# Optimization experiments

Measured on AMD Instinct MI355X. Metric: run time of the kernel, lower is better.

Reference implementation:

```python
import jax, jax.numpy as jnp
import numpy as np

B, N, K, H = 4, 1024, 48, 128
E = 128          # edge feature dim; num_in = E + H = 256
FF = 4 * H       # dense feedforward width
EPS = 1e-5
SCALE = 30.0


def gelu(x):
    return jax.nn.gelu(x, approximate=False)


def linear(x, w, b):
    # torch Linear: w is [out, in]
    return x @ w.T + b


def layer_norm(x, g, b):
    mu = jnp.mean(x, axis=-1, keepdims=True)
    var = jnp.var(x, axis=-1, keepdims=True)
    return (x - mu) * jax.lax.rsqrt(var + EPS) * g + b


def gather_nodes(nodes, idx):
    # nodes [B,N,H], idx [B,N,K] -> [B,N,K,H]
    b, n, k = idx.shape
    flat = idx.reshape(b, n * k, 1)
    return jnp.take_along_axis(nodes, flat, axis=1).reshape(b, n, k, -1)


def setup_inputs():
    key = jax.random.key(0)
    ks = jax.random.split(key, 24)
    s = 0.05
    inp = {
        "h_V": jax.random.normal(ks[0], (B, N, H), jnp.float32),
        "h_E": jax.random.normal(ks[1], (B, N, K, E), jnp.float32),
        "E_idx": jax.random.randint(ks[2], (B, N, K), 0, N, jnp.int64),
        "mask_V": jnp.ones((B, N), jnp.float32),
        "mask_attend": jnp.ones((B, N, K), jnp.float32),
        # node-update message MLP (input dim H + E + H = 3H here)
        "W1_w": jax.random.normal(ks[3], (H, H + E + H), jnp.float32) * s,
        "W1_b": jnp.zeros((H,), jnp.float32),
        "W2_w": jax.random.normal(ks[4], (H, H), jnp.float32) * s,
        "W2_b": jnp.zeros((H,), jnp.float32),
        "W3_w": jax.random.normal(ks[5], (H, H), jnp.float32) * s,
        "W3_b": jnp.zeros((H,), jnp.float32),
        # edge-update message MLP
        "W11_w": jax.random.normal(ks[6], (H, H + E + H), jnp.float32) * s,
        "W11_b": jnp.zeros((H,), jnp.float32),
        "W12_w": jax.random.normal(ks[7], (H, H), jnp.float32) * s,
        "W12_b": jnp.zeros((H,), jnp.float32),
        "W13_w": jax.random.normal(ks[8], (H, H), jnp.float32) * s,
        "W13_b": jnp.zeros((H,), jnp.float32),
        # layer norms
        "ln0_g": jnp.ones((H,), jnp.float32), "ln0_b": jnp.zeros((H,), jnp.float32),
        "ln1_g": jnp.ones((H,), jnp.float32), "ln1_b": jnp.zeros((H,), jnp.float32),
        "ln2_g": jnp.ones((H,), jnp.float32), "ln2_b": jnp.zeros((H,), jnp.float32),
        # position-wise feedforward
        "Win_w": jax.random.normal(ks[9], (FF, H), jnp.float32) * s,
        "Win_b": jnp.zeros((FF,), jnp.float32),
        "Wout_w": jax.random.normal(ks[10], (H, FF), jnp.float32) * s,
        "Wout_b": jnp.zeros((H,), jnp.float32),
        # ReZero residual weight (init 0 in the module; nonzero for testing)
        "resweight": jax.random.normal(ks[11], (1,), jnp.float32) * 0.1,
    }
    return inp


def reference(h_V, h_E, E_idx, mask_V, mask_attend,
              W1_w, W1_b, W2_w, W2_b, W3_w, W3_b,
              W11_w, W11_b, W12_w, W12_b, W13_w, W13_b,
              ln0_g, ln0_b, ln1_g, ln1_b, ln2_g, ln2_b,
              Win_w, Win_b, Wout_w, Wout_b, resweight):
    # ---- node update (pre-norm, ReZero-scaled residual), dropout=eval ----
    residual = h_V
    hVn = layer_norm(h_V, ln0_g, ln0_b)
    h_nbr = gather_nodes(hVn, E_idx)                              # [B,N,K,H]
    h_EV = jnp.concatenate(
        [jnp.broadcast_to(hVn[:, :, None, :], (B, N, K, H)), h_E, h_nbr], axis=-1)
    h_message = linear(gelu(linear(gelu(linear(h_EV, W1_w, W1_b)), W2_w, W2_b)), W3_w, W3_b)
    h_message = mask_attend[..., None] * h_message
    dh = jnp.sum(h_message, axis=-2) / SCALE
    h_V = residual + dh * resweight

    # ---- position-wise feedforward ----
    residual = h_V
    hVn = layer_norm(h_V, ln1_g, ln1_b)
    dh = linear(gelu(linear(hVn, Win_w, Win_b)), Wout_w, Wout_b)
    h_V = residual + dh * resweight
    h_V = mask_V[..., None] * h_V

    # ---- edge update (no ReZero scaling on this branch) ----
    residual = h_E
    hEn = layer_norm(h_E, ln2_g, ln2_b)
    h_nbr = gather_nodes(h_V, E_idx)
    h_EV = jnp.concatenate(
        [jnp.broadcast_to(h_V[:, :, None, :], (B, N, K, H)), hEn, h_nbr], axis=-1)
    h_message = linear(gelu(linear(gelu(linear(h_EV, W11_w, W11_b)), W12_w, W12_b)), W13_w, W13_b)
    h_E = residual + h_message

    return h_V, h_E
```

## Files before the change

kernel.cpp:

```cpp
#include <hip/hip_runtime.h>
#include <hip/hip_bf16.h>

#define BB 4
#define NN 1024
#define KK 48
#define HH 128
#define EE 128
#define IN3 384
#define FF 512
#define ST 132

typedef __attribute__((ext_vector_type(8))) short bf16x8;
typedef __attribute__((ext_vector_type(4))) float f32x4;

#define MFMA(a, b, c) __builtin_amdgcn_mfma_f32_16x16x32_bf16((a), (b), (c), 0, 0, 0)

__device__ __forceinline__ float bf2f(ushort u) {
    union { uint i; float f; } v; v.i = ((uint)u) << 16; return v.f;
}
__device__ __forceinline__ uint cvtpk(float a, float b) {
    uint r;
    asm("v_cvt_pk_bf16_f32 %0, %1, %2" : "=v"(r) : "v"(a), "v"(b));
    return r;
}
__device__ __forceinline__ ushort f2bf1(float v) {
    return (ushort)cvtpk(v, v);
}
__device__ __forceinline__ float wsum(float x) {
    #pragma unroll
    for (int o = 32; o; o >>= 1) x += __shfl_xor(x, o, 64);
    return x;
}
__device__ __forceinline__ float gelu_f(float x) {
    float t = x * fmaf(x * x, 0.044715f, 1.0f);
    float a = fminf(t * 2.3022061f, 50.0f);
    float z;
    asm("v_exp_f32 %0, %1" : "=v"(z) : "v"(a));
    float r;
    asm("v_rcp_f32 %0, %1" : "=v"(r) : "v"(z + 1.0f));
    return x * z * r;
}

__global__ __launch_bounds__(256) void k_cvt8(
    const float* __restrict__ s0, const float* __restrict__ s1,
    const float* __restrict__ s2, const float* __restrict__ s3,
    const float* __restrict__ s4, const float* __restrict__ s5,
    const float* __restrict__ s6, const float* __restrict__ s7,
    ushort* __restrict__ d0, ushort* __restrict__ d1,
    ushort* __restrict__ d2, ushort* __restrict__ d3,
    ushort* __restrict__ d4, ushort* __restrict__ d5,
    ushort* __restrict__ d6, ushort* __restrict__ d7) {
    int i = blockIdx.x * 256 + threadIdx.x;
    const float* s; ushort* d; int base;
    if      (i < 12288) { s = s0; d = d0; base = 0; }
    else if (i < 16384) { s = s1; d = d1; base = 12288; }
    else if (i < 20480) { s = s2; d = d2; base = 16384; }
    else if (i < 32768) { s = s3; d = d3; base = 20480; }
    else if (i < 36864) { s = s4; d = d4; base = 32768; }
    else if (i < 40960) { s = s5; d = d5; base = 36864; }
    else if (i < 57344) { s = s6; d = d6; base = 40960; }
    else                { s = s7; d = d7; base = 57344; }
    int j = i - base;
    float4 v = ((const float4*)s)[j];
    uint2 o;
    o.x = cvtpk(v.x, v.y);
    o.y = cvtpk(v.z, v.w);
    ((uint2*)d)[j] = o;
}

__global__ __launch_bounds__(256) void k_ln0(const float* __restrict__ hV,
                                             const float* __restrict__ g,
                                             const float* __restrict__ bta,
                                             ushort* __restrict__ out) {
    int row = blockIdx.x * 4 + (threadIdx.x >> 6);
    int l = threadIdx.x & 63;
    const float* src = hV + (size_t)row * HH;
    float x0 = src[l], x1 = src[l + 64];
    float s = wsum(x0 + x1);
    float q = wsum(x0 * x0 + x1 * x1);
    float mu = s * (1.0f / 128.0f);
    float rstd = rsqrtf(q * (1.0f / 128.0f) - mu * mu + 1e-5f);
    ushort* dst = out + (size_t)row * HH;
    dst[l]      = f2bf1((x0 - mu) * rstd * g[l]      + bta[l]);
    dst[l + 64] = f2bf1((x1 - mu) * rstd * g[l + 64] + bta[l + 64]);
}

__global__ __launch_bounds__(256, 6) void k_node(
    const float* __restrict__ hV, const float* __restrict__ hE,
    const int* __restrict__ Eidx, const float* __restrict__ maskAtt,
    const ushort* __restrict__ W1w, const float* __restrict__ W1b,
    const ushort* __restrict__ W2w, const float* __restrict__ W2b,
    const ushort* __restrict__ W3w, const float* __restrict__ W3b,
    const float* __restrict__ resw,
    const ushort* __restrict__ hVn,
    float* __restrict__ outHVp) {

    __shared__ ushort sB[KK * ST];
    __shared__ ushort sC[KK * ST];
    __shared__ float  sMask[KK];
    __shared__ float  sCol[128];

    const int t = threadIdx.x;
    const int w = t >> 6;
    const int lane = t & 63;
    const int bn = blockIdx.x;
    const int b  = bn >> 10;
    const size_t nbase = (size_t)bn * HH;
    const int r16 = lane & 15, g4 = lane >> 4;

    int myidx[3];
    #pragma unroll
    for (int mm = 0; mm < 3; mm++) myidx[mm] = Eidx[bn * KK + mm * 16 + r16];
    if (t < KK) sMask[t] = maskAtt[bn * KK + t];

    f32x4 acc[3][2];
    #pragma unroll
    for (int mm = 0; mm < 3; mm++)
        #pragma unroll
        for (int nn = 0; nn < 2; nn++) acc[mm][nn] = (f32x4){0.f, 0.f, 0.f, 0.f};

    const ushort* Wp = W1w + (w * 32 + r16) * IN3 + g4 * 8;

    {
        const ushort* nb = hVn + (size_t)b * NN * HH + g4 * 8;
        #pragma unroll
        for (int kt = 0; kt < 4; kt++) {
            bf16x8 b0 = *(const bf16x8*)(Wp + 256 + kt * 32);
            bf16x8 b1 = *(const bf16x8*)(Wp + 16 * IN3 + 256 + kt * 32);
            #pragma unroll
            for (int mm = 0; mm < 3; mm++) {
                bf16x8 a = *(const bf16x8*)(nb + (size_t)myidx[mm] * HH + kt * 32);
                acc[mm][0] = MFMA(a, b0, acc[mm][0]);
                acc[mm][1] = MFMA(a, b1, acc[mm][1]);
            }
        }
    }
    {
        const float* hEp = hE + (size_t)bn * KK * EE;
        #pragma unroll
        for (int kt = 0; kt < 4; kt++) {
            bf16x8 b0 = *(const bf16x8*)(Wp + 128 + kt * 32);
            bf16x8 b1 = *(const bf16x8*)(Wp + 16 * IN3 + 128 + kt * 32);
            #pragma unroll
            for (int mm = 0; mm < 3; mm++) {
                const float* p = hEp + (mm * 16 + r16) * EE + kt * 32 + g4 * 8;
                float4 f0 = *(const float4*)(p);
                float4 f1 = *(const float4*)(p + 4);
                union { uint u[4]; bf16x8 v; } a;
                a.u[0] = cvtpk(f0.x, f0.y); a.u[1] = cvtpk(f0.z, f0.w);
                a.u[2] = cvtpk(f1.x, f1.y); a.u[3] = cvtpk(f1.z, f1.w);
                acc[mm][0] = MFMA(a.v, b0, acc[mm][0]);
                acc[mm][1] = MFMA(a.v, b1, acc[mm][1]);
            }
        }
    }
    {
        const ushort* sp = hVn + nbase + g4 * 8;
        #pragma unroll
        for (int kt = 0; kt < 4; kt++) {
            bf16x8 aself = *(const bf16x8*)(sp + kt * 32);
            bf16x8 b0 = *(const bf16x8*)(Wp + kt * 32);
            bf16x8 b1 = *(const bf16x8*)(Wp + 16 * IN3 + kt * 32);
            #pragma unroll
            for (int mm = 0; mm < 3; mm++) {
                acc[mm][0] = MFMA(aself, b0, acc[mm][0]);
                acc[mm][1] = MFMA(aself, b1, acc[mm][1]);
            }
        }
    }
    #pragma unroll
    for (int nn = 0; nn < 2; nn++) {
        int col = w * 32 + nn * 16 + r16;
        float bb = W1b[col];
        #pragma unroll
        for (int mm = 0; mm < 3; mm++)
            #pragma unroll
            for (int r = 0; r < 4; r++)
                sB[(mm * 16 + g4 * 4 + r) * ST + col] = f2bf1(gelu_f(acc[mm][nn][r] + bb));
    }
    __syncthreads();

    f32x4 acc2[3][2];
    #pragma unroll
    for (int mm = 0; mm < 3; mm++)
        #pragma unroll
        for (int nn = 0; nn < 2; nn++) acc2[mm][nn] = (f32x4){0.f, 0.f, 0.f, 0.f};
    {
        const ushort* Wp2 = W2w + (w * 32 + r16) * HH + g4 * 8;
        #pragma unroll
        for (int kt = 0; kt < 4; kt++) {
            bf16x8 b0 = *(const bf16x8*)(Wp2 + kt * 32);
            bf16x8 b1 = *(const bf16x8*)(Wp2 + 16 * HH + kt * 32);
            #pragma unroll
            for (int mm = 0; mm < 3; mm++) {
                bf16x8 a = *(const bf16x8*)&sB[(mm * 16 + r16) * ST + kt * 32 + g4 * 8];
                acc2[mm][0] = MFMA(a, b0, acc2[mm][0]);
                acc2[mm][1] = MFMA(a, b1, acc2[mm][1]);
            }
        }
    }
    #pragma unroll
    for (int nn = 0; nn < 2; nn++) {
        int col = w * 32 + nn * 16 + r16;
        float bb = W2b[col];
        #pragma unroll
        for (int mm = 0; mm < 3; mm++)
            #pragma unroll
            for (int r = 0; r < 4; r++)
                sC[(mm * 16 + g4 * 4 + r) * ST + col] = f2bf1(gelu_f(acc2[mm][nn][r] + bb));
    }
    __syncthreads();

    f32x4 acc3[3][2];
    #pragma unroll
    for (int mm = 0; mm < 3; mm++)
        #pragma unroll
        for (int nn = 0; nn < 2; nn++) acc3[mm][nn] = (f32x4){0.f, 0.f, 0.f, 0.f};
    {
        const ushort* Wp3 = W3w + (w * 32 + r16) * HH + g4 * 8;
        #pragma unroll
        for (int kt = 0; kt < 4; kt++) {
            bf16x8 b0 = *(const bf16x8*)(Wp3 + kt * 32);
            bf16x8 b1 = *(const bf16x8*)(Wp3 + 16 * HH + kt * 32);
            #pragma unroll
            for (int mm = 0; mm < 3; mm++) {
                bf16x8 a = *(const bf16x8*)&sC[(mm * 16 + r16) * ST + kt * 32 + g4 * 8];
                acc3[mm][0] = MFMA(a, b0, acc3[mm][0]);
                acc3[mm][1] = MFMA(a, b1, acc3[mm][1]);
            }
        }
    }
    {
        float b3a = W3b[w * 32 + r16];
        float b3b = W3b[w * 32 + 16 + r16];
        float s0 = 0.f, s1 = 0.f;
        #pragma unroll
        for (int mm = 0; mm < 3; mm++)
            #pragma unroll
            for (int r = 0; r < 4; r++) {
                float mk = sMask[mm * 16 + g4 * 4 + r];
                s0 += (acc3[mm][0][r] + b3a) * mk;
                s1 += (acc3[mm][1][r] + b3b) * mk;
            }
        s0 += __shfl_xor(s0, 16, 64); s0 += __shfl_xor(s0, 32, 64);
        s1 += __shfl_xor(s1, 16, 64); s1 += __shfl_xor(s1, 32, 64);
        if (g4 == 0) {
            sCol[w * 32 + r16]      = s0;
            sCol[w * 32 + 16 + r16] = s1;
        }
    }
    __syncthreads();

    if (t < 128) {
        float rw = resw[0];
        outHVp[nbase + t] = hV[nbase + t] + sCol[t] * (1.0f / 30.0f) * rw;
    }
}

__global__ __launch_bounds__(256, 4) void k_ffn(
    const float* __restrict__ maskV,
    const float* __restrict__ ln1g, const float* __restrict__ ln1b,
    const ushort* __restrict__ Winw, const float* __restrict__ Winb,
    const ushort* __restrict__ Woutw, const float* __restrict__ Woutb,
    const float* __restrict__ resw,
    const float* __restrict__ hVp,
    float* __restrict__ outV,
    ushort* __restrict__ hV2b) {

    __shared__ float  sHVp[16 * 132];
    __shared__ ushort sX[16 * 136];
    __shared__ ushort sY[16 * 520];
    __shared__ float  sMk[16];

    const int t = threadIdx.x;
    const int w = t >> 6;
    const int lane = t & 63;
    const int nb = blockIdx.x * 16;
    const int r16 = lane & 15, g4 = lane >> 4;

    #pragma unroll
    for (int i = 0; i < 8; i++) {
        int e = t + i * 256;
        sHVp[(e >> 7) * 132 + (e & 127)] = hVp[(size_t)nb * HH + e];
    }
    if (t < 16) sMk[t] = maskV[nb + t];
    __syncthreads();

    #pragma unroll
    for (int i = 0; i < 4; i++) {
        int row = w * 4 + i;
        float x0 = sHVp[row * 132 + lane], x1 = sHVp[row * 132 + 64 + lane];
        float s = wsum(x0 + x1);
        float q = wsum(x0 * x0 + x1 * x1);
        float mu = s * (1.0f / 128.0f);
        float rstd = rsqrtf(q * (1.0f / 128.0f) - mu * mu + 1e-5f);
        sX[row * 136 + lane]      = f2bf1((x0 - mu) * rstd * ln1g[lane]      + ln1b[lane]);
        sX[row * 136 + 64 + lane] = f2bf1((x1 - mu) * rstd * ln1g[64 + lane] + ln1b[64 + lane]);
    }
    __syncthreads();

    f32x4 acc1[8];
    #pragma unroll
    for (int nn = 0; nn < 8; nn++) acc1[nn] = (f32x4){0.f, 0.f, 0.f, 0.f};
    bf16x8 a1[4];
    #pragma unroll
    for (int kt = 0; kt < 4; kt++)
        a1[kt] = *(const bf16x8*)&sX[r16 * 136 + kt * 32 + g4 * 8];
    #pragma unroll
    for (int nn = 0; nn < 8; nn++) {
        const ushort* Wq = Winw + (w * 128 + nn * 16 + r16) * HH + g4 * 8;
        #pragma unroll
        for (int kt = 0; kt < 4; kt++)
            acc1[nn] = MFMA(a1[kt], *(const bf16x8*)(Wq + kt * 32), acc1[nn]);
    }
    #pragma unroll
    for (int nn = 0; nn < 8; nn++) {
        int col = w * 128 + nn * 16 + r16;
        float bb = Winb[col];
        #pragma unroll
        for (int r = 0; r < 4; r++)
            sY[(g4 * 4 + r) * 520 + col] = f2bf1(gelu_f(acc1[nn][r] + bb));
    }
    __syncthreads();

    f32x4 acc2[2];
    acc2[0] = (f32x4){0.f, 0.f, 0.f, 0.f};
    acc2[1] = (f32x4){0.f, 0.f, 0.f, 0.f};
    {
        const ushort* Wq = Woutw + (w * 32 + r16) * FF + g4 * 8;
        #pragma unroll 4
        for (int kt = 0; kt < 16; kt++) {
            bf16x8 a = *(const bf16x8*)&sY[r16 * 520 + kt * 32 + g4 * 8];
            acc2[0] = MFMA(a, *(const bf16x8*)(Wq + kt * 32), acc2[0]);
            acc2[1] = MFMA(a, *(const bf16x8*)(Wq + 16 * FF + kt * 32), acc2[1]);
        }
    }
    float rw = resw[0];
    #pragma unroll
    for (int nn = 0; nn < 2; nn++) {
        int col = w * 32 + nn * 16 + r16;
        float bb = Woutb[col];
        #pragma unroll
        for (int r = 0; r < 4; r++) {
            int row = g4 * 4 + r;
            float out = sHVp[row * 132 + col] + (acc2[nn][r] + bb) * rw;
            out *= sMk[row];
            outV[(size_t)(nb + row) * HH + col] = out;
            hV2b[(size_t)(nb + row) * HH + col] = f2bf1(out);
        }
    }
}

__global__ __launch_bounds__(256, 6) void k_edge(
    const float* __restrict__ hE, const int* __restrict__ Eidx,
    const ushort* __restrict__ W11w, const float* __restrict__ W11b,
    const ushort* __restrict__ W12w, const float* __restrict__ W12b,
    const ushort* __restrict__ W13w, const float* __restrict__ W13b,
    const float* __restrict__ ln2g, const float* __restrict__ ln2b,
    const ushort* __restrict__ hV2b,
    float* __restrict__ outE) {

    __shared__ ushort sM[KK * ST];
    __shared__ ushort sB[KK * ST];

    const int t = threadIdx.x;
    const int w = t >> 6;
    const int lane = t & 63;
    const int bn = blockIdx.x;
    const int b  = bn >> 10;
    const size_t nbase = (size_t)bn * HH;
    const size_t ebase = (size_t)bn * KK * EE;
    const int r16 = lane & 15, g4 = lane >> 4;

    int myidx[3];
    #pragma unroll
    for (int mm = 0; mm < 3; mm++) myidx[mm] = Eidx[bn * KK + mm * 16 + r16];

    {
        float g0 = ln2g[2 * lane], g1 = ln2g[2 * lane + 1];
        float c0 = ln2b[2 * lane], c1 = ln2b[2 * lane + 1];
        #pragma unroll 3
        for (int i = 0; i < 12; i++) {
            int k = w + i * 4;
            float2 pr = ((const float2*)(hE + ebase + (size_t)k * EE))[lane];
            float x0 = pr.x, x1 = pr.y;
            float s = wsum(x0 + x1);
            float q = wsum(x0 * x0 + x1 * x1);
            float mu = s * (1.0f / 128.0f);
            float rstd = rsqrtf(q * (1.0f / 128.0f) - mu * mu + 1e-5f);
            uint packed = cvtpk((x0 - mu) * rstd * g0 + c0, (x1 - mu) * rstd * g1 + c1);
            *(uint*)&sM[k * ST + 2 * lane] = packed;
        }
    }
    __syncthreads();

    f32x4 acc[3][2];
    #pragma unroll
    for (int mm = 0; mm < 3; mm++)
        #pragma unroll
        for (int nn = 0; nn < 2; nn++) acc[mm][nn] = (f32x4){0.f, 0.f, 0.f, 0.f};

    const ushort* Wp = W11w + (w * 32 + r16) * IN3 + g4 * 8;
    {
        const ushort* nb = hV2b + (size_t)b * NN * HH + g4 * 8;
        #pragma unroll
        for (int kt = 0; kt < 4; kt++) {
            bf16x8 b0 = *(const bf16x8*)(Wp + 256 + kt * 32);
            bf16x8 b1 = *(const bf16x8*)(Wp + 16 * IN3 + 256 + kt * 32);
            #pragma unroll
            for (int mm = 0; mm < 3; mm++) {
                bf16x8 a = *(const bf16x8*)(nb + (size_t)myidx[mm] * HH + kt * 32);
                acc[mm][0] = MFMA(a, b0, acc[mm][0]);
                acc[mm][1] = MFMA(a, b1, acc[mm][1]);
            }
        }
    }
    {
        const ushort* sp = hV2b + nbase + g4 * 8;
        #pragma unroll
        for (int kt = 0; kt < 4; kt++) {
            bf16x8 aself = *(const bf16x8*)(sp + kt * 32);
            bf16x8 b0 = *(const bf16x8*)(Wp + kt * 32);
            bf16x8 b1 = *(const bf16x8*)(Wp + 16 * IN3 + kt * 32);
            #pragma unroll
            for (int mm = 0; mm < 3; mm++) {
                acc[mm][0] = MFMA(aself, b0, acc[mm][0]);
                acc[mm][1] = MFMA(aself, b1, acc[mm][1]);
            }
        }
    }
    #pragma unroll
    for (int kt = 0; kt < 4; kt++) {
        bf16x8 b0 = *(const bf16x8*)(Wp + 128 + kt * 32);
        bf16x8 b1 = *(const bf16x8*)(Wp + 16 * IN3 + 128 + kt * 32);
        #pragma unroll
        for (int mm = 0; mm < 3; mm++) {
            bf16x8 a = *(const bf16x8*)&sM[(mm * 16 + r16) * ST + kt * 32 + g4 * 8];
            acc[mm][0] = MFMA(a, b0, acc[mm][0]);
            acc[mm][1] = MFMA(a, b1, acc[mm][1]);
        }
    }
    #pragma unroll
    for (int nn = 0; nn < 2; nn++) {
        int col = w * 32 + nn * 16 + r16;
        float bb = W11b[col];
        #pragma unroll
        for (int mm = 0; mm < 3; mm++)
            #pragma unroll
            for (int r = 0; r < 4; r++)
                sB[(mm * 16 + g4 * 4 + r) * ST + col] = f2bf1(gelu_f(acc[mm][nn][r] + bb));
    }
    __syncthreads();

    f32x4 acc2[3][2];
    #pragma unroll
    for (int mm = 0; mm < 3; mm++)
        #pragma unroll
        for (int nn = 0; nn < 2; nn++) acc2[mm][nn] = (f32x4){0.f, 0.f, 0.f, 0.f};
    {
        const ushort* Wp2 = W12w + (w * 32 + r16) * HH + g4 * 8;
        #pragma unroll
        for (int kt = 0; kt < 4; kt++) {
            bf16x8 b0 = *(const bf16x8*)(Wp2 + kt * 32);
            bf16x8 b1 = *(const bf16x8*)(Wp2 + 16 * HH + kt * 32);
            #pragma unroll
            for (int mm = 0; mm < 3; mm++) {
                bf16x8 a = *(const bf16x8*)&sB[(mm * 16 + r16) * ST + kt * 32 + g4 * 8];
                acc2[mm][0] = MFMA(a, b0, acc2[mm][0]);
                acc2[mm][1] = MFMA(a, b1, acc2[mm][1]);
            }
        }
    }
    #pragma unroll
    for (int nn = 0; nn < 2; nn++) {
        int col = w * 32 + nn * 16 + r16;
        float bb = W12b[col];
        #pragma unroll
        for (int mm = 0; mm < 3; mm++)
            #pragma unroll
            for (int r = 0; r < 4; r++)
                sM[(mm * 16 + g4 * 4 + r) * ST + col] = f2bf1(gelu_f(acc2[mm][nn][r] + bb));
    }
    __syncthreads();

    f32x4 acc3[3][2];
    #pragma unroll
    for (int mm = 0; mm < 3; mm++)
        #pragma unroll
        for (int nn = 0; nn < 2; nn++) acc3[mm][nn] = (f32x4){0.f, 0.f, 0.f, 0.f};
    {
        const ushort* Wp3 = W13w + (w * 32 + r16) * HH + g4 * 8;
        #pragma unroll
        for (int kt = 0; kt < 4; kt++) {
            bf16x8 b0 = *(const bf16x8*)(Wp3 + kt * 32);
            bf16x8 b1 = *(const bf16x8*)(Wp3 + 16 * HH + kt * 32);
            #pragma unroll
            for (int mm = 0; mm < 3; mm++) {
                bf16x8 a = *(const bf16x8*)&sM[(mm * 16 + r16) * ST + kt * 32 + g4 * 8];
                acc3[mm][0] = MFMA(a, b0, acc3[mm][0]);
                acc3[mm][1] = MFMA(a, b1, acc3[mm][1]);
            }
        }
    }
    #pragma unroll
    for (int nn = 0; nn < 2; nn++) {
        int col = w * 32 + nn * 16 + r16;
        float bb = W13b[col];
        #pragma unroll
        for (int mm = 0; mm < 3; mm++)
            #pragma unroll
            for (int r = 0; r < 4; r++)
                sB[(mm * 16 + g4 * 4 + r) * ST + col] = f2bf1(acc3[mm][nn][r] + bb);
    }
    __syncthreads();

    {
        const float4* esrc = (const float4*)(hE + ebase);
        float4* edst = (float4*)(outE + ebase);
        #pragma unroll
        for (int i = 0; i < 6; i++) {
            int c = t + i * 256;
            int k = c >> 5, cp = (c & 31) * 4;
            float4 ev = esrc[c];
            const ushort* mrow = &sB[k * ST + cp];
            float4 ov;
            ov.x = ev.x + bf2f(mrow[0]);
            ov.y = ev.y + bf2f(mrow[1]);
            ov.z = ev.z + bf2f(mrow[2]);
            ov.w = ev.w + bf2f(mrow[3]);
            edst[c] = ov;
        }
    }
}

extern "C" void kernel_launch(void* const* d_in, const int* in_sizes, int n_in,
                              void* d_out, int out_size, void* d_ws, size_t ws_size,
                              hipStream_t stream) {
    const float* hV      = (const float*)d_in[0];
    const float* hE      = (const float*)d_in[1];
    const int*   Eidx    = (const int*)d_in[2];
    const float* maskV   = (const float*)d_in[3];
    const float* maskAtt = (const float*)d_in[4];
    const float* W1w  = (const float*)d_in[5];
    const float* W1b  = (const float*)d_in[6];
    const float* W2w  = (const float*)d_in[7];
    const float* W2b  = (const float*)d_in[8];
    const float* W3w  = (const float*)d_in[9];
    const float* W3b  = (const float*)d_in[10];
    const float* W11w = (const float*)d_in[11];
    const float* W11b = (const float*)d_in[12];
    const float* W12w = (const float*)d_in[13];
    const float* W12b = (const float*)d_in[14];
    const float* W13w = (const float*)d_in[15];
    const float* W13b = (const float*)d_in[16];
    const float* ln0g = (const float*)d_in[17];
    const float* ln0b = (const float*)d_in[18];
    const float* ln1g = (const float*)d_in[19];
    const float* ln1b = (const float*)d_in[20];
    const float* ln2g = (const float*)d_in[21];
    const float* ln2b = (const float*)d_in[22];
    const float* Winw  = (const float*)d_in[23];
    const float* Winb  = (const float*)d_in[24];
    const float* Woutw = (const float*)d_in[25];
    const float* Woutb = (const float*)d_in[26];
    const float* resw  = (const float*)d_in[27];

    float* outV = (float*)d_out;
    float* outE = outV + (size_t)BB * NN * HH;

    char* wsb = (char*)d_ws;
    ushort* wsHVn = (ushort*)wsb;
    float*  wHVp  = (float*)(wsb + (1 << 20));
    ushort* wHV2b = (ushort*)(wsb + 3 * (1 << 20));
    ushort* wW1   = (ushort*)(wsb + 4 * (1 << 20));
    ushort* wW2   = wW1  + HH * IN3;
    ushort* wW3   = wW2  + HH * HH;
    ushort* wW11  = wW3  + HH * HH;
    ushort* wW12  = wW11 + HH * IN3;
    ushort* wW13  = wW12 + HH * HH;
    ushort* wWin  = wW13 + HH * HH;
    ushort* wWout = wWin + FF * HH;

    k_cvt8<<<dim3(288), dim3(256), 0, stream>>>(
        W1w, W2w, W3w, W11w, W12w, W13w, Winw, Woutw,
        wW1, wW2, wW3, wW11, wW12, wW13, wWin, wWout);

    k_ln0<<<dim3(BB * NN / 4), dim3(256), 0, stream>>>(hV, ln0g, ln0b, wsHVn);
    k_node<<<dim3(BB * NN), dim3(256), 0, stream>>>(
        hV, hE, Eidx, maskAtt,
        wW1, W1b, wW2, W2b, wW3, W3b, resw, wsHVn, wHVp);
    k_ffn<<<dim3(BB * NN / 16), dim3(256), 0, stream>>>(
        maskV, ln1g, ln1b, wWin, Winb, wWout, Woutb, resw, wHVp, outV, wHV2b);
    k_edge<<<dim3(BB * NN), dim3(256), 0, stream>>>(
        hE, Eidx, wW11, W11b, wW12, W12b, wW13, W13b,
        ln2g, ln2b, wHV2b, outE);
}
```

Before: 281.9 us.

## Process two nodes per block in node and edge kernels with shared LDS buffer

Each block of k_node and k_edge now handles two nodes (96 edge rows) instead of one, so every weight fragment loaded from global memory feeds twice as many MFMAs. The two LDS staging buffers are merged into one buffer that is reused in place, with extra barriers added. The edge kernel's final residual add now writes directly from registers to global memory instead of staging through LDS. Costs include doubled accumulator register pressure, lower launch-bounds occupancy (4 blocks instead of 6), half as many blocks, and strided scalar global stores in the edge epilogue.

```diff
diff --git a/kernel.cpp b/kernel.cpp
--- a/kernel.cpp
+++ b/kernel.cpp
@@ -85,7 +85,7 @@
     dst[l + 64] = f2bf1((x1 - mu) * rstd * g[l + 64] + bta[l + 64]);
 }
 
-__global__ __launch_bounds__(256, 6) void k_node(
+__global__ __launch_bounds__(256, 4) void k_node(
     const float* __restrict__ hV, const float* __restrict__ hE,
     const int* __restrict__ Eidx, const float* __restrict__ maskAtt,
     const ushort* __restrict__ W1w, const float* __restrict__ W1b,
@@ -95,32 +95,49 @@
     const ushort* __restrict__ hVn,
     float* __restrict__ outHVp) {
 
-    __shared__ ushort sB[KK * ST];
-    __shared__ ushort sC[KK * ST];
-    __shared__ float  sMask[KK];
-    __shared__ float  sCol[128];
+    __shared__ ushort buf[96 * ST];
+    __shared__ float  sMask[96];
+    __shared__ float  sCol[256];
 
     const int t = threadIdx.x;
     const int w = t >> 6;
     const int lane = t & 63;
-    const int bn = blockIdx.x;
-    const int b  = bn >> 10;
-    const size_t nbase = (size_t)bn * HH;
+    const int np = blockIdx.x * 2;
+    const int b  = np >> 10;
     const int r16 = lane & 15, g4 = lane >> 4;
 
-    int myidx[3];
-    #pragma unroll
-    for (int mm = 0; mm < 3; mm++) myidx[mm] = Eidx[bn * KK + mm * 16 + r16];
-    if (t < KK) sMask[t] = maskAtt[bn * KK + t];
-
-    f32x4 acc[3][2];
-    #pragma unroll
-    for (int mm = 0; mm < 3; mm++)
-        #pragma unroll
-        for (int nn = 0; nn < 2; nn++) acc[mm][nn] = (f32x4){0.f, 0.f, 0.f, 0.f};
-
-    const ushort* Wp = W1w + (w * 32 + r16) * IN3 + g4 * 8;
-
+    int myidx[6];
+    #pragma unroll
+    for (int mt = 0; mt < 6; mt++)
+        myidx[mt] = Eidx[np * KK + mt * 16 + r16];
+    if (t < 96) sMask[t] = maskAtt[np * KK + t];
+
+    f32x4 acc[6][2];
+    #pragma unroll
+    for (int mt = 0; mt < 6; mt++) {
+        acc[mt][0] = (f32x4){0.f, 0.f, 0.f, 0.f};
+        acc[mt][1] = (f32x4){0.f, 0.f, 0.f, 0.f};
+    }
+
+    const ushort* Wp  = W1w + (w * 32 + r16) * IN3 + g4 * 8;
+    const float*  hE0 = hE + (size_t)np * KK * EE;
+
+    #pragma unroll
+    for (int kt = 0; kt < 4; kt++) {
+        bf16x8 b0 = *(const bf16x8*)(Wp + 128 + kt * 32);
+        bf16x8 b1 = *(const bf16x8*)(Wp + 16 * IN3 + 128 + kt * 32);
+        #pragma unroll
+        for (int mt = 0; mt < 6; mt++) {
+            const float* p = hE0 + (size_t)(mt * 16 + r16) * EE + kt * 32 + g4 * 8;
+            float4 f0 = *(const float4*)(p);
+            float4 f1 = *(const float4*)(p + 4);
+            union { uint u[4]; bf16x8 v; } a;
+            a.u[0] = cvtpk(f0.x, f0.y); a.u[1] = cvtpk(f0.z, f0.w);
+            a.u[2] = cvtpk(f1.x, f1.y); a.u[3] = cvtpk(f1.z, f1.w);
+            acc[mt][0] = MFMA(a.v, b0, acc[mt][0]);
+            acc[mt][1] = MFMA(a.v, b1, acc[mt][1]);
+        }
+    }
     {
         const ushort* nb = hVn + (size_t)b * NN * HH + g4 * 8;
         #pragma unroll
@@ -128,43 +145,27 @@
             bf16x8 b0 = *(const bf16x8*)(Wp + 256 + kt * 32);
             bf16x8 b1 = *(const bf16x8*)(Wp + 16 * IN3 + 256 + kt * 32);
             #pragma unroll
-            for (int mm = 0; mm < 3; mm++) {
-                bf16x8 a = *(const bf16x8*)(nb + (size_t)myidx[mm] * HH + kt * 32);
-                acc[mm][0] = MFMA(a, b0, acc[mm][0]);
-                acc[mm][1] = MFMA(a, b1, acc[mm][1]);
-            }
-        }
-    }
-    {
-        const float* hEp = hE + (size_t)bn * KK * EE;
-        #pragma unroll
-        for (int kt = 0; kt < 4; kt++) {
-            bf16x8 b0 = *(const bf16x8*)(Wp + 128 + kt * 32);
-            bf16x8 b1 = *(const bf16x8*)(Wp + 16 * IN3 + 128 + kt * 32);
-            #pragma unroll
-            for (int mm = 0; mm < 3; mm++) {
-                const float* p = hEp + (mm * 16 + r16) * EE + kt * 32 + g4 * 8;
-                float4 f0 = *(const float4*)(p);
-                float4 f1 = *(const float4*)(p + 4);
-                union { uint u[4]; bf16x8 v; } a;
-                a.u[0] = cvtpk(f0.x, f0.y); a.u[1] = cvtpk(f0.z, f0.w);
-                a.u[2] = cvtpk(f1.x, f1.y); a.u[3] = cvtpk(f1.z, f1.w);
-                acc[mm][0] = MFMA(a.v, b0, acc[mm][0]);
-                acc[mm][1] = MFMA(a.v, b1, acc[mm][1]);
-            }
-        }
-    }
-    {
-        const ushort* sp = hVn + nbase + g4 * 8;
-        #pragma unroll
-        for (int kt = 0; kt < 4; kt++) {
-            bf16x8 aself = *(const bf16x8*)(sp + kt * 32);
+            for (int mt = 0; mt < 6; mt++) {
+                bf16x8 a = *(const bf16x8*)(nb + (size_t)myidx[mt] * HH + kt * 32);
+                acc[mt][0] = MFMA(a, b0, acc[mt][0]);
+                acc[mt][1] = MFMA(a, b1, acc[mt][1]);
+            }
+        }
+    }
+    {
+        const ushort* sp0 = hVn + (size_t)np * HH + g4 * 8;
+        const ushort* sp1 = sp0 + HH;
+        #pragma unroll
+        for (int kt = 0; kt < 4; kt++) {
+            bf16x8 a0 = *(const bf16x8*)(sp0 + kt * 32);
+            bf16x8 a1 = *(const bf16x8*)(sp1 + kt * 32);
             bf16x8 b0 = *(const bf16x8*)(Wp + kt * 32);
             bf16x8 b1 = *(const bf16x8*)(Wp + 16 * IN3 + kt * 32);
             #pragma unroll
-            for (int mm = 0; mm < 3; mm++) {
-                acc[mm][0] = MFMA(aself, b0, acc[mm][0]);
-                acc[mm][1] = MFMA(aself, b1, acc[mm][1]);
+            for (int mt = 0; mt < 6; mt++) {
+                bf16x8 a = (mt < 3) ? a0 : a1;
+                acc[mt][0] = MFMA(a, b0, acc[mt][0]);
+                acc[mt][1] = MFMA(a, b1, acc[mt][1]);
             }
         }
     }
@@ -173,18 +174,19 @@
         int col = w * 32 + nn * 16 + r16;
         float bb = W1b[col];
         #pragma unroll
-        for (int mm = 0; mm < 3; mm++)
+        for (int mt = 0; mt < 6; mt++)
             #pragma unroll
             for (int r = 0; r < 4; r++)
-                sB[(mm * 16 + g4 * 4 + r) * ST + col] = f2bf1(gelu_f(acc[mm][nn][r] + bb));
-    }
-    __syncthreads();
-
-    f32x4 acc2[3][2];
-    #pragma unroll
-    for (int mm = 0; mm < 3; mm++)
-        #pragma unroll
-        for (int nn = 0; nn < 2; nn++) acc2[mm][nn] = (f32x4){0.f, 0.f, 0.f, 0.f};
+                buf[(mt * 16 + g4 * 4 + r) * ST + col] = f2bf1(gelu_f(acc[mt][nn][r] + bb));
+    }
+    __syncthreads();
+
+    f32x4 acc2[6][2];
+    #pragma unroll
+    for (int mt = 0; mt < 6; mt++) {
+        acc2[mt][0] = (f32x4){0.f, 0.f, 0.f, 0.f};
+        acc2[mt][1] = (f32x4){0.f, 0.f, 0.f, 0.f};
+    }
     {
         const ushort* Wp2 = W2w + (w * 32 + r16) * HH + g4 * 8;
         #pragma unroll
@@ -192,30 +194,32 @@
             bf16x8 b0 = *(const bf16x8*)(Wp2 + kt * 32);
             bf16x8 b1 = *(const bf16x8*)(Wp2 + 16 * HH + kt * 32);
             #pragma unroll
-            for (int mm = 0; mm < 3; mm++) {
-                bf16x8 a = *(const bf16x8*)&sB[(mm * 16 + r16) * ST + kt * 32 + g4 * 8];
-                acc2[mm][0] = MFMA(a, b0, acc2[mm][0]);
-                acc2[mm][1] = MFMA(a, b1, acc2[mm][1]);
-            }
-        }
-    }
+            for (int mt = 0; mt < 6; mt++) {
+                bf16x8 a = *(const bf16x8*)&buf[(mt * 16 + r16) * ST + kt * 32 + g4 * 8];
+                acc2[mt][0] = MFMA(a, b0, acc2[mt][0]);
+                acc2[mt][1] = MFMA(a, b1, acc2[mt][1]);
+            }
+        }
+    }
+    __syncthreads();
     #pragma unroll
     for (int nn = 0; nn < 2; nn++) {
         int col = w * 32 + nn * 16 + r16;
         float bb = W2b[col];
         #pragma unroll
-        for (int mm = 0; mm < 3; mm++)
+        for (int mt = 0; mt < 6; mt++)
             #pragma unroll
             for (int r = 0; r < 4; r++)
-                sC[(mm * 16 + g4 * 4 + r) * ST + col] = f2bf1(gelu_f(acc2[mm][nn][r] + bb));
-    }
-    __syncthreads();
-
-    f32x4 acc3[3][2];
-    #pragma unroll
-    for (int mm = 0; mm < 3; mm++)
-        #pragma unroll
-        for (int nn = 0; nn < 2; nn++) acc3[mm][nn] = (f32x4){0.f, 0.f, 0.f, 0.f};
+                buf[(mt * 16 + g4 * 4 + r) * ST + col] = f2bf1(gelu_f(acc2[mt][nn][r] + bb));
+    }
+    __syncthreads();
+
+    f32x4 acc3[6][2];
+    #pragma unroll
+    for (int mt = 0; mt < 6; mt++) {
+        acc3[mt][0] = (f32x4){0.f, 0.f, 0.f, 0.f};
+        acc3[mt][1] = (f32x4){0.f, 0.f, 0.f, 0.f};
+    }
     {
         const ushort* Wp3 = W3w + (w * 32 + r16) * HH + g4 * 8;
         #pragma unroll
@@ -223,37 +227,45 @@
             bf16x8 b0 = *(const bf16x8*)(Wp3 + kt * 32);
             bf16x8 b1 = *(const bf16x8*)(Wp3 + 16 * HH + kt * 32);
             #pragma unroll
-            for (int mm = 0; mm < 3; mm++) {
-                bf16x8 a = *(const bf16x8*)&sC[(mm * 16 + r16) * ST + kt * 32 + g4 * 8];
-                acc3[mm][0] = MFMA(a, b0, acc3[mm][0]);
-                acc3[mm][1] = MFMA(a, b1, acc3[mm][1]);
+            for (int mt = 0; mt < 6; mt++) {
+                bf16x8 a = *(const bf16x8*)&buf[(mt * 16 + r16) * ST + kt * 32 + g4 * 8];
+                acc3[mt][0] = MFMA(a, b0, acc3[mt][0]);
+                acc3[mt][1] = MFMA(a, b1, acc3[mt][1]);
             }
         }
     }
     {
         float b3a = W3b[w * 32 + r16];
         float b3b = W3b[w * 32 + 16 + r16];
-        float s0 = 0.f, s1 = 0.f;
-        #pragma unroll
-        for (int mm = 0; mm < 3; mm++)
+        float s0a = 0.f, s0b = 0.f, s1a = 0.f, s1b = 0.f;
+        #pragma unroll
+        for (int mt = 0; mt < 6; mt++)
             #pragma unroll
             for (int r = 0; r < 4; r++) {
-                float mk = sMask[mm * 16 + g4 * 4 + r];
-                s0 += (acc3[mm][0][r] + b3a) * mk;
-                s1 += (acc3[mm][1][r] + b3b) * mk;
-            }
-        s0 += __shfl_xor(s0, 16, 64); s0 += __shfl_xor(s0, 32, 64);
-        s1 += __shfl_xor(s1, 16, 64); s1 += __shfl_xor(s1, 32, 64);
+                int row = mt * 16 + g4 * 4 + r;
+                float mk = sMask[row];
+                float v0 = (acc3[mt][0][r] + b3a) * mk;
+                float v1 = (acc3[mt][1][r] + b3b) * mk;
+                if (mt < 3) { s0a += v0; s0b += v1; }
+                else        { s1a += v0; s1b += v1; }
+            }
+        s0a += __shfl_xor(s0a, 16, 64); s0a += __shfl_xor(s0a, 32, 64);
+        s0b += __shfl_xor(s0b, 16, 64); s0b += __shfl_xor(s0b, 32, 64);
+        s1a += __shfl_xor(s1a, 16, 64); s1a += __shfl_xor(s1a, 32, 64);
+        s1b += __shfl_xor(s1b, 16, 64); s1b += __shfl_xor(s1b, 32, 64);
         if (g4 == 0) {
-            sCol[w * 32 + r16]      = s0;
-            sCol[w * 32 + 16 + r16] = s1;
-        }
-    }
-    __syncthreads();
-
-    if (t < 128) {
+            sCol[w * 32 + r16]            = s0a;
+            sCol[w * 32 + 16 + r16]       = s0b;
+            sCol[128 + w * 32 + r16]      = s1a;
+            sCol[128 + w * 32 + 16 + r16] = s1b;
+        }
+    }
+    __syncthreads();
+
+    {
         float rw = resw[0];
-        outHVp[nbase + t] = hV[nbase + t] + sCol[t] * (1.0f / 30.0f) * rw;
+        size_t o = (size_t)np * HH + t;
+        outHVp[o] = hV[o] + sCol[t] * (1.0f / 30.0f) * rw;
     }
 }
 
@@ -351,7 +363,7 @@
     }
 }
 
-__global__ __launch_bounds__(256, 6) void k_edge(
+__global__ __launch_bounds__(256, 4) void k_edge(
     const float* __restrict__ hE, const int* __restrict__ Eidx,
     const ushort* __restrict__ W11w, const float* __restrict__ W11b,
     const ushort* __restrict__ W12w, const float* __restrict__ W12b,
@@ -360,46 +372,45 @@
     const ushort* __restrict__ hV2b,
     float* __restrict__ outE) {
 
-    __shared__ ushort sM[KK * ST];
-    __shared__ ushort sB[KK * ST];
+    __shared__ ushort buf[96 * ST];
 
     const int t = threadIdx.x;
     const int w = t >> 6;
     const int lane = t & 63;
-    const int bn = blockIdx.x;
-    const int b  = bn >> 10;
-    const size_t nbase = (size_t)bn * HH;
-    const size_t ebase = (size_t)bn * KK * EE;
+    const int np = blockIdx.x * 2;
+    const int b  = np >> 10;
+    const size_t eb = (size_t)np * KK * EE;
     const int r16 = lane & 15, g4 = lane >> 4;
 
-    int myidx[3];
-    #pragma unroll
-    for (int mm = 0; mm < 3; mm++) myidx[mm] = Eidx[bn * KK + mm * 16 + r16];
+    int myidx[6];
+    #pragma unroll
+    for (int mt = 0; mt < 6; mt++)
+        myidx[mt] = Eidx[np * KK + mt * 16 + r16];
 
     {
         float g0 = ln2g[2 * lane], g1 = ln2g[2 * lane + 1];
         float c0 = ln2b[2 * lane], c1 = ln2b[2 * lane + 1];
-        #pragma unroll 3
-        for (int i = 0; i < 12; i++) {
+        #pragma unroll 4
+        for (int i = 0; i < 24; i++) {
             int k = w + i * 4;
-            float2 pr = ((const float2*)(hE + ebase + (size_t)k * EE))[lane];
+            float2 pr = ((const float2*)(hE + eb + (size_t)k * EE))[lane];
             float x0 = pr.x, x1 = pr.y;
             float s = wsum(x0 + x1);
             float q = wsum(x0 * x0 + x1 * x1);
             float mu = s * (1.0f / 128.0f);
             float rstd = rsqrtf(q * (1.0f / 128.0f) - mu * mu + 1e-5f);
             uint packed = cvtpk((x0 - mu) * rstd * g0 + c0, (x1 - mu) * rstd * g1 + c1);
-            *(uint*)&sM[k * ST + 2 * lane] = packed;
-        }
-    }
-    __syncthreads();
-
-    f32x4 acc[3][2];
-    #pragma unroll
-    for (int mm = 0; mm < 3; mm++)
-        #pragma unroll
-        for (int nn = 0; nn < 2; nn++) acc[mm][nn] = (f32x4){0.f, 0.f, 0.f, 0.f};
-
+            *(uint*)&buf[k * ST + 2 * lane] = packed;
+        }
+    }
+    __syncthreads();
+
+    f32x4 acc[6][2];
+    #pragma unroll
+    for (int mt = 0; mt < 6; mt++) {
+        acc[mt][0] = (f32x4){0.f, 0.f, 0.f, 0.f};
+        acc[mt][1] = (f32x4){0.f, 0.f, 0.f, 0.f};
+    }
     const ushort* Wp = W11w + (w * 32 + r16) * IN3 + g4 * 8;
     {
         const ushort* nb = hV2b + (size_t)b * NN * HH + g4 * 8;
@@ -408,24 +419,10 @@
             bf16x8 b0 = *(const bf16x8*)(Wp + 256 + kt * 32);
             bf16x8 b1 = *(const bf16x8*)(Wp + 16 * IN3 + 256 + kt * 32);
             #pragma unroll
-            for (int mm = 0; mm < 3; mm++) {
-                bf16x8 a = *(const bf16x8*)(nb + (size_t)myidx[mm] * HH + kt * 32);
-                acc[mm][0] = MFMA(a, b0, acc[mm][0]);
-                acc[mm][1] = MFMA(a, b1, acc[mm][1]);
-            }
-        }
-    }
-    {
-        const ushort* sp = hV2b + nbase + g4 * 8;
-        #pragma unroll
-        for (int kt = 0; kt < 4; kt++) {
-            bf16x8 aself = *(const bf16x8*)(sp + kt * 32);
-            bf16x8 b0 = *(const bf16x8*)(Wp + kt * 32);
-            bf16x8 b1 = *(const bf16x8*)(Wp + 16 * IN3 + kt * 32);
-            #pragma unroll
-            for (int mm = 0; mm < 3; mm++) {
-                acc[mm][0] = MFMA(aself, b0, acc[mm][0]);
-                acc[mm][1] = MFMA(aself, b1, acc[mm][1]);
+            for (int mt = 0; mt < 6; mt++) {
+                bf16x8 a = *(const bf16x8*)(nb + (size_t)myidx[mt] * HH + kt * 32);
+                acc[mt][0] = MFMA(a, b0, acc[mt][0]);
+                acc[mt][1] = MFMA(a, b1, acc[mt][1]);
             }
         }
     }
@@ -434,29 +431,48 @@
         bf16x8 b0 = *(const bf16x8*)(Wp + 128 + kt * 32);
         bf16x8 b1 = *(const bf16x8*)(Wp + 16 * IN3 + 128 + kt * 32);
         #pragma unroll
-        for (int mm = 0; mm < 3; mm++) {
-            bf16x8 a = *(const bf16x8*)&sM[(mm * 16 + r16) * ST + kt * 32 + g4 * 8];
-            acc[mm][0] = MFMA(a, b0, acc[mm][0]);
-            acc[mm][1] = MFMA(a, b1, acc[mm][1]);
-        }
-    }
+        for (int mt = 0; mt < 6; mt++) {
+            bf16x8 a = *(const bf16x8*)&buf[(mt * 16 + r16) * ST + kt * 32 + g4 * 8];
+            acc[mt][0] = MFMA(a, b0, acc[mt][0]);
+            acc[mt][1] = MFMA(a, b1, acc[mt][1]);
+        }
+    }
+    {
+        const ushort* sp0 = hV2b + (size_t)np * HH + g4 * 8;
+        const ushort* sp1 = sp0 + HH;
+        #pragma unroll
+        for (int kt = 0; kt < 4; kt++) {
+            bf16x8 a0 = *(const bf16x8*)(sp0 + kt * 32);
+            bf16x8 a1s = *(const bf16x8*)(sp1 + kt * 32);
+            bf16x8 b0 = *(const bf16x8*)(Wp + kt * 32);
+            bf16x8 b1 = *(const bf16x8*)(Wp + 16 * IN3 + kt * 32);
+            #pragma unroll
+            for (int mt = 0; mt < 6; mt++) {
+                bf16x8 a = (mt < 3) ? a0 : a1s;
+                acc[mt][0] = MFMA(a, b0, acc[mt][0]);
+                acc[mt][1] = MFMA(a, b1, acc[mt][1]);
+            }
+        }
+    }
+    __syncthreads();
     #pragma unroll
     for (int nn = 0; nn < 2; nn++) {
         int col = w * 32 + nn * 16 + r16;
         float bb = W11b[col];
         #pragma unroll
-        for (int mm = 0; mm < 3; mm++)
+        for (int mt = 0; mt < 6; mt++)
             #pragma unroll
             for (int r = 0; r < 4; r++)
-                sB[(mm * 16 + g4 * 4 + r) * ST + col] = f2bf1(gelu_f(acc[mm][nn][r] + bb));
-    }
-    __syncthreads();
-
-    f32x4 acc2[3][2];
-    #pragma unroll
-    for (int mm = 0; mm < 3; mm++)
-        #pragma unroll
-        for (int nn = 0; nn < 2; nn++) acc2[mm][nn] = (f32x4){0.f, 0.f, 0.f, 0.f};
+                buf[(mt * 16 + g4 * 4 + r) * ST + col] = f2bf1(gelu_f(acc[mt][nn][r] + bb));
+    }
+    __syncthreads();
+
+    f32x4 acc2[6][2];
+    #pragma unroll
+    for (int mt = 0; mt < 6; mt++) {
+        acc2[mt][0] = (f32x4){0.f, 0.f, 0.f, 0.f};
+        acc2[mt][1] = (f32x4){0.f, 0.f, 0.f, 0.f};
+    }
     {
         const ushort* Wp2 = W12w + (w * 32 + r16) * HH + g4 * 8;
         #pragma unroll
@@ -464,30 +480,32 @@
             bf16x8 b0 = *(const bf16x8*)(Wp2 + kt * 32);
             bf16x8 b1 = *(const bf16x8*)(Wp2 + 16 * HH + kt * 32);
             #pragma unroll
-            for (int mm = 0; mm < 3; mm++) {
-                bf16x8 a = *(const bf16x8*)&sB[(mm * 16 + r16) * ST + kt * 32 + g4 * 8];
-                acc2[mm][0] = MFMA(a, b0, acc2[mm][0]);
-                acc2[mm][1] = MFMA(a, b1, acc2[mm][1]);
-            }
-        }
-    }
+            for (int mt = 0; mt < 6; mt++) {
+                bf16x8 a = *(const bf16x8*)&buf[(mt * 16 + r16) * ST + kt * 32 + g4 * 8];
+                acc2[mt][0] = MFMA(a, b0, acc2[mt][0]);
+                acc2[mt][1] = MFMA(a, b1, acc2[mt][1]);
+            }
+        }
+    }
+    __syncthreads();
     #pragma unroll
     for (int nn = 0; nn < 2; nn++) {
         int col = w * 32 + nn * 16 + r16;
         float bb = W12b[col];
         #pragma unroll
-        for (int mm = 0; mm < 3; mm++)
+        for (int mt = 0; mt < 6; mt++)
             #pragma unroll
             for (int r = 0; r < 4; r++)
-                sM[(mm * 16 + g4 * 4 + r) * ST + col] = f2bf1(gelu_f(acc2[mm][nn][r] + bb));
-    }
-    __syncthreads();
-
-    f32x4 acc3[3][2];
-    #pragma unroll
-    for (int mm = 0; mm < 3; mm++)
-        #pragma unroll
-        for (int nn = 0; nn < 2; nn++) acc3[mm][nn] = (f32x4){0.f, 0.f, 0.f, 0.f};
+                buf[(mt * 16 + g4 * 4 + r) * ST + col] = f2bf1(gelu_f(acc2[mt][nn][r] + bb));
+    }
+    __syncthreads();
+
+    f32x4 acc3[6][2];
+    #pragma unroll
+    for (int mt = 0; mt < 6; mt++) {
+        acc3[mt][0] = (f32x4){0.f, 0.f, 0.f, 0.f};
+        acc3[mt][1] = (f32x4){0.f, 0.f, 0.f, 0.f};
+    }
     {
         const ushort* Wp3 = W13w + (w * 32 + r16) * HH + g4 * 8;
         #pragma unroll
@@ -495,10 +513,10 @@
             bf16x8 b0 = *(const bf16x8*)(Wp3 + kt * 32);
             bf16x8 b1 = *(const bf16x8*)(Wp3 + 16 * HH + kt * 32);
             #pragma unroll
-            for (int mm = 0; mm < 3; mm++) {
-                bf16x8 a = *(const bf16x8*)&sM[(mm * 16 + r16) * ST + kt * 32 + g4 * 8];
-                acc3[mm][0] = MFMA(a, b0, acc3[mm][0]);
-                acc3[mm][1] = MFMA(a, b1, acc3[mm][1]);
+            for (int mt = 0; mt < 6; mt++) {
+                bf16x8 a = *(const bf16x8*)&buf[(mt * 16 + r16) * ST + kt * 32 + g4 * 8];
+                acc3[mt][0] = MFMA(a, b0, acc3[mt][0]);
+                acc3[mt][1] = MFMA(a, b1, acc3[mt][1]);
             }
         }
     }
@@ -507,29 +525,13 @@
         int col = w * 32 + nn * 16 + r16;
         float bb = W13b[col];
         #pragma unroll
-        for (int mm = 0; mm < 3; mm++)
-            #pragma unroll
-            for (int r = 0; r < 4; r++)
-                sB[(mm * 16 + g4 * 4 + r) * ST + col] = f2bf1(acc3[mm][nn][r] + bb);
-    }
-    __syncthreads();
-
-    {
-        const float4* esrc = (const float4*)(hE + ebase);
-        float4* edst = (float4*)(outE + ebase);
-        #pragma unroll
-        for (int i = 0; i < 6; i++) {
-            int c = t + i * 256;
-            int k = c >> 5, cp = (c & 31) * 4;
-            float4 ev = esrc[c];
-            const ushort* mrow = &sB[k * ST + cp];
-            float4 ov;
-            ov.x = ev.x + bf2f(mrow[0]);
-            ov.y = ev.y + bf2f(mrow[1]);
-            ov.z = ev.z + bf2f(mrow[2]);
-            ov.w = ev.w + bf2f(mrow[3]);
-            edst[c] = ov;
-        }
+        for (int mt = 0; mt < 6; mt++)
+            #pragma unroll
+            for (int r = 0; r < 4; r++) {
+                int row = mt * 16 + g4 * 4 + r;
+                size_t off = eb + (size_t)row * EE + col;
+                outE[off] = hE[off] + acc3[mt][nn][r] + bb;
+            }
     }
 }
 
@@ -586,12 +588,12 @@
         wW1, wW2, wW3, wW11, wW12, wW13, wWin, wWout);
 
     k_ln0<<<dim3(BB * NN / 4), dim3(256), 0, stream>>>(hV, ln0g, ln0b, wsHVn);
-    k_node<<<dim3(BB * NN), dim3(256), 0, stream>>>(
+    k_node<<<dim3(BB * NN / 2), dim3(256), 0, stream>>>(
         hV, hE, Eidx, maskAtt,
         wW1, W1b, wW2, W2b, wW3, W3b, resw, wsHVn, wHVp);
     k_ffn<<<dim3(BB * NN / 16), dim3(256), 0, stream>>>(
         maskV, ln1g, ln1b, wWin, Winb, wWout, Woutb, resw, wHVp, outV, wHV2b);
-    k_edge<<<dim3(BB * NN), dim3(256), 0, stream>>>(
+    k_edge<<<dim3(BB * NN / 2), dim3(256), 0, stream>>>(
         hE, Eidx, wW11, W11b, wW12, W12b, wW13, W13b,
         ln2g, ln2b, wHV2b, outE);
 }
```

Measured after the change: 250.7 us, median of 2. 1.12x faster.
